# Kernel optimization log

Hardware: AMD Instinct MI355X
Metric: run time of the kernel (lower is better)

## Reference

```python
import jax, jax.numpy as jnp
import numpy as np

LOG2 = float(np.log(2.0))

def ssp(x):
    # shifted softplus used by SchNet
    return jax.nn.softplus(x) - LOG2

def setup_inputs() -> dict:
    key = jax.random.key(0)
    k1, k2, k3, k4, k5 = jax.random.split(key, 5)
    N, E, D, F = 100000, 600000, 128, 64
    nodes = jax.random.normal(k1, (N, D), dtype=jnp.float32)
    edges = jax.random.normal(k2, (E, F), dtype=jnp.float32)
    edges_i = jax.random.randint(k3, (E, 2), 0, N, dtype=jnp.int64)
    W1 = jax.random.normal(k4, (F, D), dtype=jnp.float32) * (1.0 / np.sqrt(F))
    b1 = jnp.zeros((D,), dtype=jnp.float32)
    W2 = jax.random.normal(k5, (D, D), dtype=jnp.float32) * (1.0 / np.sqrt(D))
    b2 = jnp.zeros((D,), dtype=jnp.float32)
    return {"nodes": nodes, "edges": edges, "edges_i": edges_i,
            "W1": W1, "b1": b1, "W2": W2, "b2": b2}

def reference(nodes, edges, edges_i, W1, b1, W2, b2):
    starts = edges_i[:, 0]  # [E]
    ends = edges_i[:, 1]    # [E]
    # edge MLP filter: two Dense layers with shifted-softplus
    filt = ssp(edges @ W1 + b1)   # [E, D]
    filt = ssp(filt @ W2 + b2)    # [E, D]
    # gather end nodes, modulate by filter, scatter-add onto start nodes
    msgs = nodes[ends] * filt     # [E, D]
    return nodes.at[starts].add(msgs)  # [N, D]
```

## Files before the change

kernel.cpp:

```cpp
#include <hip/hip_runtime.h>
#include <math.h>

#define DD 128
#define FF 64
#define BM 64
#define SENT 0xFFFFFFFFu

typedef __attribute__((ext_vector_type(8))) short bf16x8;
typedef __attribute__((ext_vector_type(4))) short short4s;
typedef __attribute__((ext_vector_type(4))) float f32x4;

__device__ __forceinline__ float ssp_f(float x) {
    float ax = fabsf(x);
    float e  = __expf(-ax);
    return fmaxf(x, 0.0f) + __logf(1.0f + e) - 0.6931471805599453f;
}

__device__ __forceinline__ unsigned short f2bf(float f) {
    unsigned u = __float_as_uint(f);
    unsigned r = (u + 0x7FFFu + ((u >> 16) & 1u)) >> 16;
    return (unsigned short)r;
}
__device__ __forceinline__ float bf2f(unsigned short h) {
    return __uint_as_float(((unsigned)h) << 16);
}

__global__ void copy_nodes_kernel(const float4* __restrict__ src,
                                  float4* __restrict__ dst, int n4) {
    int i = blockIdx.x * blockDim.x + threadIdx.x;
    int stride = gridDim.x * blockDim.x;
    for (; i < n4; i += stride) dst[i] = src[i];
}

__global__ void zero_u32_kernel(unsigned* __restrict__ p, int n) {
    int i = blockIdx.x * blockDim.x + threadIdx.x;
    int stride = gridDim.x * blockDim.x;
    for (; i < n; i += stride) p[i] = 0u;
}

__global__ void hist_kernel(const int* __restrict__ eidx,
                            unsigned* __restrict__ counts, int E) {
    int e = blockIdx.x * blockDim.x + threadIdx.x;
    if (e < E) atomicAdd(&counts[eidx[2 * e]], 1u);
}

__global__ void scan1_kernel(const unsigned* __restrict__ counts,
                             unsigned* __restrict__ cursor,
                             unsigned* __restrict__ bsums, int n) {
    __shared__ unsigned s[256];
    int i = blockIdx.x * 256 + threadIdx.x;
    unsigned v = (i < n) ? counts[i] : 0u;
    s[threadIdx.x] = v;
    __syncthreads();
    #pragma unroll
    for (int d = 1; d < 256; d <<= 1) {
        unsigned t = (threadIdx.x >= d) ? s[threadIdx.x - d] : 0u;
        __syncthreads();
        s[threadIdx.x] += t;
        __syncthreads();
    }
    if (i < n) cursor[i] = s[threadIdx.x] - v;
    if (threadIdx.x == 255) bsums[blockIdx.x] = s[255];
}

__global__ void scan2_kernel(unsigned* __restrict__ bsums, int nb) {
    __shared__ unsigned s[512];
    int t = threadIdx.x;
    if (nb <= 512) {
        unsigned v = (t < nb) ? bsums[t] : 0u;
        s[t] = v;
        __syncthreads();
        #pragma unroll
        for (int d = 1; d < 512; d <<= 1) {
            unsigned x = (t >= d) ? s[t - d] : 0u;
            __syncthreads();
            s[t] += x;
            __syncthreads();
        }
        if (t < nb) bsums[t] = s[t] - v;
    } else if (t == 0) {
        unsigned run = 0u;
        for (int i = 0; i < nb; ++i) { unsigned x = bsums[i]; bsums[i] = run; run += x; }
    }
}

__global__ void scan3_kernel(unsigned* __restrict__ cursor,
                             const unsigned* __restrict__ bsums, int n) {
    int i = blockIdx.x * 256 + threadIdx.x;
    if (i < n) cursor[i] += bsums[blockIdx.x];
}

__global__ void scatter_ids_kernel(const int* __restrict__ eidx,
                                   unsigned* __restrict__ cursor,
                                   unsigned* __restrict__ sorted_e,
                                   unsigned* __restrict__ sorted_nt,
                                   unsigned* __restrict__ sorted_ns, int E) {
    int e = blockIdx.x * blockDim.x + threadIdx.x;
    if (e < E) {
        int ns = eidx[2 * e];
        unsigned pos = atomicAdd(&cursor[ns], 1u);
        sorted_e[pos]  = (unsigned)e;
        sorted_nt[pos] = (unsigned)eidx[2 * e + 1];
        sorted_ns[pos] = (unsigned)ns;
    }
}

__global__ void prep_w_kernel(const float* __restrict__ W, int K,
                              unsigned short* __restrict__ hi,
                              unsigned short* __restrict__ lo) {
    int S = K >> 5;
    int idx = blockIdx.x * blockDim.x + threadIdx.x;
    int total = 8 * S * 64;
    if (idx >= total) return;
    int l = idx & 63;
    int s = (idx >> 6) % S;
    int j = idx / (64 * S);
    int col = j * 16 + (l & 15);
    int kbase = s * 32 + (l >> 4) * 8;
    int ob = ((j * S + s) * 64 + l) * 8;
    #pragma unroll
    for (int i = 0; i < 8; ++i) {
        float w = W[(size_t)(kbase + i) * DD + col];
        unsigned short h = f2bf(w);
        hi[ob + i] = h;
        lo[ob + i] = f2bf(w - bf2f(h));
    }
}

__launch_bounds__(256, 4)
__global__ void edge_mfma_kernel(const float* __restrict__ nodes,
                                 const float* __restrict__ edges,
                                 const unsigned* __restrict__ sorted_e,
                                 const unsigned* __restrict__ sorted_nt,
                                 const unsigned* __restrict__ sorted_ns,
                                 const unsigned* __restrict__ ends,
                                 const unsigned short* __restrict__ W1h,
                                 const unsigned short* __restrict__ W1l,
                                 const unsigned short* __restrict__ W2h,
                                 const unsigned short* __restrict__ W2l,
                                 const float* __restrict__ b1,
                                 const float* __restrict__ b2,
                                 float* __restrict__ out,
                                 float* __restrict__ bpart,
                                 unsigned* __restrict__ bnode,
                                 int E) {
    __shared__ unsigned short region[16384];
    float* SM = reinterpret_cast<float*>(region);

    const int t = threadIdx.x;
    const int tlo = blockIdx.x * BM;

    unsigned ns_reg = (tlo + (t & 63) < E) ? sorted_ns[tlo + (t & 63)] : SENT;

    const float4* e4 = reinterpret_cast<const float4*>(edges);
    #pragma unroll
    for (int it = 0; it < 4; ++it) {
        int idx = it * 256 + t;
        int row = idx >> 4, c4 = idx & 15;
        int i = tlo + row;
        float4 v = make_float4(0.f, 0.f, 0.f, 0.f);
        if (i < E) {
            unsigned e = sorted_e[i];
            v = e4[(size_t)e * (FF / 4) + c4];
        }
        short4s hv = { (short)f2bf(v.x), (short)f2bf(v.y),
                       (short)f2bf(v.z), (short)f2bf(v.w) };
        int g = c4 >> 1, half = c4 & 1;
        *reinterpret_cast<short4s*>(region + row * FF +
            ((g ^ (row & 7)) * 8) + half * 4) = hv;
    }
    __syncthreads();

    const int lane = t & 63, wave = t >> 6;
    const int wrow = wave * 16;
    const int lr = lane & 15, lg = lane >> 4;
    const f32x4 zero4 = { 0.f, 0.f, 0.f, 0.f };

    bf16x8 a1[2];
    #pragma unroll
    for (int s = 0; s < 2; ++s) {
        int row = wrow + lr;
        a1[s] = *reinterpret_cast<const bf16x8*>(
            region + row * FF + (((s * 4 + lg) ^ (row & 7)) * 8));
    }
    __syncthreads();

    f32x4 acc1[8];
    #pragma unroll
    for (int j = 0; j < 8; ++j) acc1[j] = zero4;
    #pragma unroll
    for (int j = 0; j < 8; ++j) {
        bf16x8 wh[2], wl[2];
        #pragma unroll
        for (int s = 0; s < 2; ++s) {
            wh[s] = *reinterpret_cast<const bf16x8*>(W1h + ((size_t)((j * 2 + s) * 64 + lane)) * 8);
            wl[s] = *reinterpret_cast<const bf16x8*>(W1l + ((size_t)((j * 2 + s) * 64 + lane)) * 8);
        }
        #pragma unroll
        for (int s = 0; s < 2; ++s) {
            acc1[j] = __builtin_amdgcn_mfma_f32_16x16x32_bf16(a1[s], wh[s], acc1[j], 0, 0, 0);
            acc1[j] = __builtin_amdgcn_mfma_f32_16x16x32_bf16(a1[s], wl[s], acc1[j], 0, 0, 0);
        }
    }

    #pragma unroll
    for (int j = 0; j < 8; ++j) {
        int col = j * 16 + lr;
        float bv = b1[col];
        int gc = col >> 3, ci = col & 7;
        #pragma unroll
        for (int r = 0; r < 4; ++r) {
            int row = wrow + lg * 4 + r;
            region[row * DD + ((gc ^ (row & 15)) * 8 + ci)] =
                f2bf(ssp_f(acc1[j][r] + bv));
        }
    }
    __syncthreads();

    bf16x8 a2[4];
    #pragma unroll
    for (int s = 0; s < 4; ++s) {
        int row = wrow + lr;
        a2[s] = *reinterpret_cast<const bf16x8*>(
            region + row * DD + (((s * 4 + lg) ^ (row & 15)) * 8));
    }
    __syncthreads();

    float4 nv[8];
    const float4* n4 = reinterpret_cast<const float4*>(nodes);
    #pragma unroll
    for (int it = 0; it < 8; ++it) {
        int idx = it * 256 + t;
        int row = idx >> 5, c4 = idx & 31;
        unsigned nt_ = (tlo + row < E) ? sorted_nt[tlo + row] : 0u;
        nv[it] = n4[(size_t)nt_ * 32 + c4];
    }

    f32x4 acc2[8];
    #pragma unroll
    for (int j = 0; j < 8; ++j) acc2[j] = zero4;
    #pragma unroll
    for (int j = 0; j < 8; ++j) {
        bf16x8 wh[4], wl[4];
        #pragma unroll
        for (int s = 0; s < 4; ++s) {
            wh[s] = *reinterpret_cast<const bf16x8*>(W2h + ((size_t)((j * 4 + s) * 64 + lane)) * 8);
            wl[s] = *reinterpret_cast<const bf16x8*>(W2l + ((size_t)((j * 4 + s) * 64 + lane)) * 8);
        }
        #pragma unroll
        for (int s = 0; s < 4; ++s) {
            acc2[j] = __builtin_amdgcn_mfma_f32_16x16x32_bf16(a2[s], wh[s], acc2[j], 0, 0, 0);
            acc2[j] = __builtin_amdgcn_mfma_f32_16x16x32_bf16(a2[s], wl[s], acc2[j], 0, 0, 0);
        }
    }

    #pragma unroll
    for (int j = 0; j < 8; ++j) {
        int col = j * 16 + lr;
        float bv = b2[col];
        #pragma unroll
        for (int r = 0; r < 4; ++r) {
            int row = wrow + lg * 4 + r;
            SM[row * DD + (col ^ ((row & 7) << 2))] = ssp_f(acc2[j][r] + bv);
        }
    }
    __syncthreads();

    #pragma unroll
    for (int it = 0; it < 8; ++it) {
        int idx = it * 256 + t;
        int row = idx >> 5, c4 = idx & 31;
        int foff = row * DD + ((c4 * 4) ^ ((row & 7) << 2));
        float4 mv = *reinterpret_cast<float4*>(SM + foff);
        mv.x *= nv[it].x; mv.y *= nv[it].y; mv.z *= nv[it].z; mv.w *= nv[it].w;
        *reinterpret_cast<float4*>(SM + foff) = mv;
    }
    __syncthreads();

    if (t < DD) {
        const int col = t;
        unsigned n0 = __shfl(ns_reg, 0);
        unsigned s0 = (n0 == 0u) ? 0u : ends[n0 - 1];
        bool contFirst = (s0 < (unsigned)tlo);
        if (t == 0) bnode[blockIdx.x] = contFirst ? n0 : SENT;

        float acc = 0.f;
        unsigned cur = n0;
        int segstart = 0;
        #pragma unroll 1
        for (int r = 0; r < BM; ++r) {
            unsigned n = __shfl(ns_reg, r);
            if (n != cur) {
                if (segstart == 0 && contFirst)
                    bpart[(size_t)blockIdx.x * DD + col] = acc;
                else
                    out[(size_t)cur * DD + col] = nodes[(size_t)cur * DD + col] + acc;
                cur = n; acc = 0.f; segstart = r;
            }
            acc += SM[r * DD + (col ^ ((r & 7) << 2))];
        }
        if (cur != SENT) {
            if (segstart == 0 && contFirst)
                bpart[(size_t)blockIdx.x * DD + col] = acc;
            else
                out[(size_t)cur * DD + col] = nodes[(size_t)cur * DD + col] + acc;
        }
    }
}

__global__ void fixup_bpart_kernel(const float* __restrict__ bpart,
                                   const unsigned* __restrict__ bnode,
                                   float* __restrict__ out, int NT) {
    int ti = blockIdx.x * 2 + (threadIdx.x >> 7);
    if (ti >= NT) return;
    unsigned n = bnode[ti];
    if (n == SENT) return;
    int c = threadIdx.x & 127;
    atomicAdd(&out[(size_t)n * DD + c], bpart[(size_t)ti * DD + c]);
}

__global__ void copy_empty_kernel(const unsigned* __restrict__ counts,
                                  const float4* __restrict__ nodes4,
                                  float4* __restrict__ out4, int N) {
    int n = blockIdx.x * 8 + (threadIdx.x >> 5);
    if (n >= N) return;
    if (counts[n] != 0u) return;
    int d4 = threadIdx.x & 31;
    out4[(size_t)n * 32 + d4] = nodes4[(size_t)n * 32 + d4];
}

__launch_bounds__(256, 2)
__global__ void edge_fused_atomic_kernel(const float* __restrict__ nodes,
                                         const float* __restrict__ edges,
                                         const int*   __restrict__ eidx,
                                         const float* __restrict__ W1,
                                         const float* __restrict__ b1,
                                         const float* __restrict__ W2,
                                         const float* __restrict__ b2,
                                         float* __restrict__ out, int E) {
    int e = blockIdx.x * 256 + threadIdx.x;
    if (e >= E) return;
    int ns = eidx[2 * e + 0];
    int nt = eidx[2 * e + 1];

    float h1[DD];
    #pragma unroll
    for (int d = 0; d < DD; ++d) h1[d] = b1[d];
    const float4* ev4 = reinterpret_cast<const float4*>(edges) + (size_t)e * (FF / 4);
    #pragma unroll 1
    for (int f4 = 0; f4 < FF / 4; ++f4) {
        float4 ev = ev4[f4];
        const float* w0 = W1 + (size_t)(f4 * 4) * DD;
        #pragma unroll
        for (int d = 0; d < DD; ++d) h1[d] = fmaf(ev.x, w0[d], h1[d]);
        #pragma unroll
        for (int d = 0; d < DD; ++d) h1[d] = fmaf(ev.y, w0[DD + d], h1[d]);
        #pragma unroll
        for (int d = 0; d < DD; ++d) h1[d] = fmaf(ev.z, w0[2 * DD + d], h1[d]);
        #pragma unroll
        for (int d = 0; d < DD; ++d) h1[d] = fmaf(ev.w, w0[3 * DD + d], h1[d]);
    }
    #pragma unroll
    for (int d = 0; d < DD; ++d) h1[d] = ssp_f(h1[d]);

    const float* nrow = nodes + (size_t)nt * DD;
    float*       orow = out   + (size_t)ns * DD;
    #pragma unroll 1
    for (int c = 0; c < 2; ++c) {
        const int base = c * 64;
        float h2[64];
        #pragma unroll
        for (int j = 0; j < 64; ++j) h2[j] = b2[base + j];
        #pragma unroll
        for (int k = 0; k < DD; ++k) {
            float hk = h1[k];
            const float* w = W2 + (size_t)k * DD + base;
            #pragma unroll
            for (int j = 0; j < 64; ++j) h2[j] = fmaf(hk, w[j], h2[j]);
        }
        #pragma unroll
        for (int j = 0; j < 64; ++j) {
            float m = ssp_f(h2[j]) * nrow[base + j];
            __hip_atomic_fetch_add(&orow[base + j], m,
                                   __ATOMIC_RELAXED, __HIP_MEMORY_SCOPE_AGENT);
        }
    }
}

extern "C" void kernel_launch(void* const* d_in, const int* in_sizes, int n_in,
                              void* d_out, int out_size, void* d_ws, size_t ws_size,
                              hipStream_t stream) {
    const float* nodes = (const float*)d_in[0];
    const float* edges = (const float*)d_in[1];
    const int*   eidx  = (const int*)  d_in[2];
    const float* W1    = (const float*)d_in[3];
    const float* b1    = (const float*)d_in[4];
    const float* W2    = (const float*)d_in[5];
    const float* b2    = (const float*)d_in[6];
    float* out = (float*)d_out;

    int ND = in_sizes[0];
    int N  = ND / DD;
    int E  = in_sizes[1] / FF;
    int NT = (E + BM - 1) / BM;

    int nb = (N + 255) / 256;
    uintptr_t base = (uintptr_t)d_ws;
    uintptr_t p = base;
    unsigned* counts    = (unsigned*)p;  p += (size_t)N * 4;
    unsigned* cursor    = (unsigned*)p;  p += (size_t)N * 4;
    unsigned* bsums     = (unsigned*)p;  p += (size_t)nb * 4;
    unsigned* sorted_e  = (unsigned*)p;  p += (size_t)E * 4;
    unsigned* sorted_nt = (unsigned*)p;  p += (size_t)E * 4;
    unsigned* sorted_ns = (unsigned*)p;  p += (size_t)E * 4;
    p = (p + 255) & ~(uintptr_t)255;
    unsigned short* W1h = (unsigned short*)p;  p += (size_t)FF * DD * 2;
    unsigned short* W1l = (unsigned short*)p;  p += (size_t)FF * DD * 2;
    unsigned short* W2h = (unsigned short*)p;  p += (size_t)DD * DD * 2;
    unsigned short* W2l = (unsigned short*)p;  p += (size_t)DD * DD * 2;
    unsigned* bnode     = (unsigned*)p;  p += (size_t)NT * 4;
    p = (p + 255) & ~(uintptr_t)255;
    float* bpart        = (float*)p;     p += (size_t)NT * DD * 4;

    if ((size_t)(p - base) > ws_size) {
        copy_nodes_kernel<<<dim3(1024), dim3(256), 0, stream>>>(
            (const float4*)nodes, (float4*)out, ND / 4);
        edge_fused_atomic_kernel<<<dim3((E + 255) / 256), dim3(256), 0, stream>>>(
            nodes, edges, eidx, W1, b1, W2, b2, out, E);
        return;
    }

    prep_w_kernel<<<dim3(4), dim3(256), 0, stream>>>(W1, FF, W1h, W1l);
    prep_w_kernel<<<dim3(8), dim3(256), 0, stream>>>(W2, DD, W2h, W2l);

    zero_u32_kernel<<<dim3(256), dim3(256), 0, stream>>>(counts, N);
    hist_kernel<<<dim3((E + 255) / 256), dim3(256), 0, stream>>>(eidx, counts, E);
    scan1_kernel<<<dim3(nb), dim3(256), 0, stream>>>(counts, cursor, bsums, N);
    scan2_kernel<<<dim3(1), dim3(512), 0, stream>>>(bsums, nb);
    scan3_kernel<<<dim3(nb), dim3(256), 0, stream>>>(cursor, bsums, N);
    scatter_ids_kernel<<<dim3((E + 255) / 256), dim3(256), 0, stream>>>(
        eidx, cursor, sorted_e, sorted_nt, sorted_ns, E);

    copy_empty_kernel<<<dim3((N + 7) / 8), dim3(256), 0, stream>>>(
        counts, (const float4*)nodes, (float4*)out, N);

    edge_mfma_kernel<<<dim3(NT), dim3(256), 0, stream>>>(
        nodes, edges, sorted_e, sorted_nt, sorted_ns, cursor,
        W1h, W1l, W2h, W2l, b1, b2, out, bpart, bnode, E);

    fixup_bpart_kernel<<<dim3((NT + 1) / 2), dim3(256), 0, stream>>>(
        bpart, bnode, out, NT);
}
```

Before: 399.7 us.

## Halve LDS footprint by splitting second GEMM into column halves

The second MFMA GEMM and the scatter epilogue now run in two passes over 64-column halves, which halves the shared-memory staging buffer (32KB to 16KB) and the live accumulator and node registers. The launch-bounds occupancy hint rises from 4 to 6 blocks. The segmented row reduction is also split across 128 threads, each covering half the rows, with a shared-memory handoff for a segment that crosses the midpoint. In exchange, the extra syncthreads and passes add serialization, and the midpoint carry logic makes correctness more delicate.

```diff
diff --git a/kernel.cpp b/kernel.cpp
--- a/kernel.cpp
+++ b/kernel.cpp
@@ -127,7 +127,7 @@
     }
 }
 
-__launch_bounds__(256, 4)
+__launch_bounds__(256, 6)
 __global__ void edge_mfma_kernel(const float* __restrict__ nodes,
                                  const float* __restrict__ edges,
                                  const unsigned* __restrict__ sorted_e,
@@ -144,7 +144,8 @@
                                  float* __restrict__ bpart,
                                  unsigned* __restrict__ bnode,
                                  int E) {
-    __shared__ unsigned short region[16384];
+    __shared__ unsigned short region[8192];
+    __shared__ float comm[64];
     float* SM = reinterpret_cast<float*>(region);
 
     const int t = threadIdx.x;
@@ -226,84 +227,119 @@
     }
     __syncthreads();
 
-    float4 nv[8];
-    const float4* n4 = reinterpret_cast<const float4*>(nodes);
-    #pragma unroll
-    for (int it = 0; it < 8; ++it) {
-        int idx = it * 256 + t;
-        int row = idx >> 5, c4 = idx & 31;
-        unsigned nt_ = (tlo + row < E) ? sorted_nt[tlo + row] : 0u;
-        nv[it] = n4[(size_t)nt_ * 32 + c4];
-    }
-
-    f32x4 acc2[8];
-    #pragma unroll
-    for (int j = 0; j < 8; ++j) acc2[j] = zero4;
-    #pragma unroll
-    for (int j = 0; j < 8; ++j) {
-        bf16x8 wh[4], wl[4];
-        #pragma unroll
-        for (int s = 0; s < 4; ++s) {
-            wh[s] = *reinterpret_cast<const bf16x8*>(W2h + ((size_t)((j * 4 + s) * 64 + lane)) * 8);
-            wl[s] = *reinterpret_cast<const bf16x8*>(W2l + ((size_t)((j * 4 + s) * 64 + lane)) * 8);
-        }
-        #pragma unroll
-        for (int s = 0; s < 4; ++s) {
-            acc2[j] = __builtin_amdgcn_mfma_f32_16x16x32_bf16(a2[s], wh[s], acc2[j], 0, 0, 0);
-            acc2[j] = __builtin_amdgcn_mfma_f32_16x16x32_bf16(a2[s], wl[s], acc2[j], 0, 0, 0);
-        }
-    }
-
-    #pragma unroll
-    for (int j = 0; j < 8; ++j) {
-        int col = j * 16 + lr;
-        float bv = b2[col];
-        #pragma unroll
-        for (int r = 0; r < 4; ++r) {
-            int row = wrow + lg * 4 + r;
-            SM[row * DD + (col ^ ((row & 7) << 2))] = ssp_f(acc2[j][r] + bv);
-        }
-    }
-    __syncthreads();
-
-    #pragma unroll
-    for (int it = 0; it < 8; ++it) {
-        int idx = it * 256 + t;
-        int row = idx >> 5, c4 = idx & 31;
-        int foff = row * DD + ((c4 * 4) ^ ((row & 7) << 2));
-        float4 mv = *reinterpret_cast<float4*>(SM + foff);
-        mv.x *= nv[it].x; mv.y *= nv[it].y; mv.z *= nv[it].z; mv.w *= nv[it].w;
-        *reinterpret_cast<float4*>(SM + foff) = mv;
-    }
-    __syncthreads();
-
-    if (t < DD) {
-        const int col = t;
-        unsigned n0 = __shfl(ns_reg, 0);
-        unsigned s0 = (n0 == 0u) ? 0u : ends[n0 - 1];
-        bool contFirst = (s0 < (unsigned)tlo);
-        if (t == 0) bnode[blockIdx.x] = contFirst ? n0 : SENT;
-
-        float acc = 0.f;
-        unsigned cur = n0;
-        int segstart = 0;
-        #pragma unroll 1
-        for (int r = 0; r < BM; ++r) {
-            unsigned n = __shfl(ns_reg, r);
-            if (n != cur) {
+    unsigned n0  = __shfl(ns_reg, 0);
+    unsigned n31 = __shfl(ns_reg, 31);
+    unsigned n32 = __shfl(ns_reg, 32);
+    bool cont_mid = (n31 == n32) && (n31 != SENT);
+    unsigned s0 = (n0 == 0u) ? 0u : ends[n0 - 1];
+    bool contFirst = (s0 < (unsigned)tlo);
+    bool spans0 = (n0 == n31);
+
+    const float4* n4p = reinterpret_cast<const float4*>(nodes);
+
+    #pragma unroll 1
+    for (int h = 0; h < 2; ++h) {
+        float4 nv[4];
+        #pragma unroll
+        for (int it = 0; it < 4; ++it) {
+            int idx = it * 256 + t;
+            int row = idx >> 4, c4 = idx & 15;
+            unsigned nt_ = (tlo + row < E) ? sorted_nt[tlo + row] : 0u;
+            nv[it] = n4p[(size_t)nt_ * 32 + h * 16 + c4];
+        }
+
+        f32x4 acc2[4];
+        #pragma unroll
+        for (int jj = 0; jj < 4; ++jj) acc2[jj] = zero4;
+        #pragma unroll
+        for (int jj = 0; jj < 4; ++jj) {
+            int j = h * 4 + jj;
+            bf16x8 wh[4], wl[4];
+            #pragma unroll
+            for (int s = 0; s < 4; ++s) {
+                wh[s] = *reinterpret_cast<const bf16x8*>(W2h + ((size_t)((j * 4 + s) * 64 + lane)) * 8);
+                wl[s] = *reinterpret_cast<const bf16x8*>(W2l + ((size_t)((j * 4 + s) * 64 + lane)) * 8);
+            }
+            #pragma unroll
+            for (int s = 0; s < 4; ++s) {
+                acc2[jj] = __builtin_amdgcn_mfma_f32_16x16x32_bf16(a2[s], wh[s], acc2[jj], 0, 0, 0);
+                acc2[jj] = __builtin_amdgcn_mfma_f32_16x16x32_bf16(a2[s], wl[s], acc2[jj], 0, 0, 0);
+            }
+        }
+
+        #pragma unroll
+        for (int jj = 0; jj < 4; ++jj) {
+            int col = (h * 4 + jj) * 16 + lr;
+            float bv = b2[col];
+            int colh = jj * 16 + lr;
+            #pragma unroll
+            for (int r = 0; r < 4; ++r) {
+                int row = wrow + lg * 4 + r;
+                SM[row * 64 + (colh ^ (((row >> 2) & 3) << 4))] =
+                    ssp_f(acc2[jj][r] + bv);
+            }
+        }
+        __syncthreads();
+
+        #pragma unroll
+        for (int it = 0; it < 4; ++it) {
+            int idx = it * 256 + t;
+            int row = idx >> 4, c4 = idx & 15;
+            int foff = row * 64 + ((c4 * 4) ^ (((row >> 2) & 3) << 4));
+            float4 mv = *reinterpret_cast<float4*>(SM + foff);
+            mv.x *= nv[it].x; mv.y *= nv[it].y; mv.z *= nv[it].z; mv.w *= nv[it].w;
+            *reinterpret_cast<float4*>(SM + foff) = mv;
+        }
+        __syncthreads();
+
+        float firstacc = 0.f;
+        bool firstpend = false;
+        if (t < 128) {
+            int y  = t >> 6;
+            int cl = t & 63;
+            int col = h * 64 + cl;
+            int rbeg = y * 32;
+            float acc = 0.f;
+            unsigned cur = __shfl(ns_reg, rbeg);
+            int segstart = rbeg;
+            bool pend = (y == 1) && cont_mid;
+            #pragma unroll 1
+            for (int r = rbeg; r < rbeg + 32; ++r) {
+                unsigned n = __shfl(ns_reg, r);
+                if (n != cur) {
+                    if (pend) { firstacc = acc; firstpend = true; pend = false; }
+                    else if (cur != SENT) {
+                        if (segstart == 0 && contFirst)
+                            bpart[(size_t)blockIdx.x * DD + col] = acc;
+                        else
+                            out[(size_t)cur * DD + col] = nodes[(size_t)cur * DD + col] + acc;
+                    }
+                    cur = n; acc = 0.f; segstart = r;
+                }
+                acc += SM[r * 64 + (cl ^ (((r >> 2) & 3) << 4))];
+            }
+            if (y == 0 && cont_mid) {
+                comm[cl] = acc;
+            } else if (pend) {
+                firstacc = acc; firstpend = true;
+            } else if (cur != SENT) {
                 if (segstart == 0 && contFirst)
                     bpart[(size_t)blockIdx.x * DD + col] = acc;
                 else
                     out[(size_t)cur * DD + col] = nodes[(size_t)cur * DD + col] + acc;
-                cur = n; acc = 0.f; segstart = r;
             }
-            acc += SM[r * DD + (col ^ ((r & 7) << 2))];
-        }
-        if (cur != SENT) {
-            if (segstart == 0 && contFirst)
-                bpart[(size_t)blockIdx.x * DD + col] = acc;
+            if (t == 0 && h == 0) bnode[blockIdx.x] = contFirst ? n0 : SENT;
+        }
+        __syncthreads();
+
+        if (t >= 64 && t < 128 && firstpend) {
+            int cl = t & 63;
+            int col = h * 64 + cl;
+            float total = comm[cl] + firstacc;
+            if (spans0 && contFirst)
+                bpart[(size_t)blockIdx.x * DD + col] = total;
             else
-                out[(size_t)cur * DD + col] = nodes[(size_t)cur * DD + col] + acc;
+                out[(size_t)n31 * DD + col] = nodes[(size_t)n31 * DD + col] + total;
         }
     }
 }
```

Result: slower. 553.1 us (+38.4%).

## Materialize sorted bf16 swizzled edge rows in scatter pass for contiguous tile loads

Applied to the files above, without the earlier changes.

The scatter pass that sorts edges by start node now also converts each edge's feature row to bf16, pre-swizzles it, and writes it at its sorted position in a workspace buffer. The edge MFMA kernel then copies its 64-row tile into shared memory with two contiguous 16-byte loads per thread, instead of an indirect fp32 gather plus conversion. This removes the sorted_e indirection and the random gather latency from the main kernel. In exchange it adds a full extra write and read of the bf16 edge matrix, and tail rows past E in the last tile are left uninitialized rather than zeroed.

```diff
diff --git a/kernel.cpp b/kernel.cpp
--- a/kernel.cpp
+++ b/kernel.cpp
@@ -90,18 +90,29 @@
     if (i < n) cursor[i] += bsums[blockIdx.x];
 }
 
-__global__ void scatter_ids_kernel(const int* __restrict__ eidx,
-                                   unsigned* __restrict__ cursor,
-                                   unsigned* __restrict__ sorted_e,
-                                   unsigned* __restrict__ sorted_nt,
-                                   unsigned* __restrict__ sorted_ns, int E) {
+__global__ void scatter_move_kernel(const int* __restrict__ eidx,
+                                    const float* __restrict__ edges,
+                                    unsigned* __restrict__ cursor,
+                                    unsigned short* __restrict__ edgesS,
+                                    unsigned* __restrict__ sorted_nt,
+                                    unsigned* __restrict__ sorted_ns, int E) {
     int e = blockIdx.x * blockDim.x + threadIdx.x;
-    if (e < E) {
-        int ns = eidx[2 * e];
-        unsigned pos = atomicAdd(&cursor[ns], 1u);
-        sorted_e[pos]  = (unsigned)e;
-        sorted_nt[pos] = (unsigned)eidx[2 * e + 1];
-        sorted_ns[pos] = (unsigned)ns;
+    if (e >= E) return;
+    int ns = eidx[2 * e];
+    unsigned pos = atomicAdd(&cursor[ns], 1u);
+    sorted_nt[pos] = (unsigned)eidx[2 * e + 1];
+    sorted_ns[pos] = (unsigned)ns;
+
+    int r = (int)(pos & 63);
+    unsigned short* drow = edgesS + (size_t)pos * FF;
+    const float4* src = reinterpret_cast<const float4*>(edges) + (size_t)e * 16;
+    #pragma unroll
+    for (int q = 0; q < 16; ++q) {
+        float4 v = src[q];
+        short4s hv = { (short)f2bf(v.x), (short)f2bf(v.y),
+                       (short)f2bf(v.z), (short)f2bf(v.w) };
+        int g = q >> 1, half = q & 1;
+        *reinterpret_cast<short4s*>(drow + ((g ^ (r & 7)) * 8) + half * 4) = hv;
     }
 }
 
@@ -129,8 +140,7 @@
 
 __launch_bounds__(256, 4)
 __global__ void edge_mfma_kernel(const float* __restrict__ nodes,
-                                 const float* __restrict__ edges,
-                                 const unsigned* __restrict__ sorted_e,
+                                 const unsigned short* __restrict__ edgesS,
                                  const unsigned* __restrict__ sorted_nt,
                                  const unsigned* __restrict__ sorted_ns,
                                  const unsigned* __restrict__ ends,
@@ -152,22 +162,11 @@
 
     unsigned ns_reg = (tlo + (t & 63) < E) ? sorted_ns[tlo + (t & 63)] : SENT;
 
-    const float4* e4 = reinterpret_cast<const float4*>(edges);
-    #pragma unroll
-    for (int it = 0; it < 4; ++it) {
-        int idx = it * 256 + t;
-        int row = idx >> 4, c4 = idx & 15;
-        int i = tlo + row;
-        float4 v = make_float4(0.f, 0.f, 0.f, 0.f);
-        if (i < E) {
-            unsigned e = sorted_e[i];
-            v = e4[(size_t)e * (FF / 4) + c4];
-        }
-        short4s hv = { (short)f2bf(v.x), (short)f2bf(v.y),
-                       (short)f2bf(v.z), (short)f2bf(v.w) };
-        int g = c4 >> 1, half = c4 & 1;
-        *reinterpret_cast<short4s*>(region + row * FF +
-            ((g ^ (row & 7)) * 8) + half * 4) = hv;
+    {
+        const bf16x8* src = reinterpret_cast<const bf16x8*>(edgesS + (size_t)tlo * FF);
+        bf16x8* dst = reinterpret_cast<bf16x8*>(region);
+        dst[t]       = src[t];
+        dst[256 + t] = src[256 + t];
     }
     __syncthreads();
 
@@ -410,7 +409,6 @@
     unsigned* counts    = (unsigned*)p;  p += (size_t)N * 4;
     unsigned* cursor    = (unsigned*)p;  p += (size_t)N * 4;
     unsigned* bsums     = (unsigned*)p;  p += (size_t)nb * 4;
-    unsigned* sorted_e  = (unsigned*)p;  p += (size_t)E * 4;
     unsigned* sorted_nt = (unsigned*)p;  p += (size_t)E * 4;
     unsigned* sorted_ns = (unsigned*)p;  p += (size_t)E * 4;
     p = (p + 255) & ~(uintptr_t)255;
@@ -421,6 +419,9 @@
     unsigned* bnode     = (unsigned*)p;  p += (size_t)NT * 4;
     p = (p + 255) & ~(uintptr_t)255;
     float* bpart        = (float*)p;     p += (size_t)NT * DD * 4;
+    p = (p + 255) & ~(uintptr_t)255;
+    unsigned short* edgesS = (unsigned short*)p;
+    p += (size_t)NT * BM * FF * 2;
 
     if ((size_t)(p - base) > ws_size) {
         copy_nodes_kernel<<<dim3(1024), dim3(256), 0, stream>>>(
@@ -438,14 +439,14 @@
     scan1_kernel<<<dim3(nb), dim3(256), 0, stream>>>(counts, cursor, bsums, N);
     scan2_kernel<<<dim3(1), dim3(512), 0, stream>>>(bsums, nb);
     scan3_kernel<<<dim3(nb), dim3(256), 0, stream>>>(cursor, bsums, N);
-    scatter_ids_kernel<<<dim3((E + 255) / 256), dim3(256), 0, stream>>>(
-        eidx, cursor, sorted_e, sorted_nt, sorted_ns, E);
+    scatter_move_kernel<<<dim3((E + 255) / 256), dim3(256), 0, stream>>>(
+        eidx, edges, cursor, edgesS, sorted_nt, sorted_ns, E);
 
     copy_empty_kernel<<<dim3((N + 7) / 8), dim3(256), 0, stream>>>(
         counts, (const float4*)nodes, (float4*)out, N);
 
     edge_mfma_kernel<<<dim3(NT), dim3(256), 0, stream>>>(
-        nodes, edges, sorted_e, sorted_nt, sorted_ns, cursor,
+        nodes, edgesS, sorted_nt, sorted_ns, cursor,
         W1h, W1l, W2h, W2l, b1, b2, out, bpart, bnode, E);
 
     fixup_bpart_kernel<<<dim3((NT + 1) / 2), dim3(256), 0, stream>>>(
```

New measurement: 394.6 us. No clear change (-1.3%).
